# Kernel tuning notes

Hardware: AMD Instinct MI355X
Metric: run time of the kernel (lower is better)

## Reference

```python
import jax, jax.numpy as jnp
import numpy as np

D_MODEL = 512
NUM_HEADS = 8
HEAD_DIM = D_MODEL // NUM_HEADS
MAX_REL = 2


def setup_inputs() -> dict:
    key = jax.random.key(0)
    ks = jax.random.split(key, 12)
    B, S = 2, 4096
    std = 1.0 / np.sqrt(D_MODEL)
    inp = {
        'q': jax.random.normal(ks[0], (B, S, D_MODEL), jnp.float32),
        'k': jax.random.normal(ks[1], (B, S, D_MODEL), jnp.float32),
        'v': jax.random.normal(ks[2], (B, S, D_MODEL), jnp.float32),
        'Wq': jax.random.normal(ks[3], (D_MODEL, D_MODEL), jnp.float32) * std,
        'bq': jnp.zeros((D_MODEL,), jnp.float32),
        'Wk': jax.random.normal(ks[4], (D_MODEL, D_MODEL), jnp.float32) * std,
        'bk': jnp.zeros((D_MODEL,), jnp.float32),
        'Wv': jax.random.normal(ks[5], (D_MODEL, D_MODEL), jnp.float32) * std,
        'bv': jnp.zeros((D_MODEL,), jnp.float32),
        'Wo': jax.random.normal(ks[6], (D_MODEL, D_MODEL), jnp.float32) * std,
        'bo': jnp.zeros((D_MODEL,), jnp.float32),
        'rel_pos': jax.random.normal(ks[7], (NUM_HEADS, 2 * MAX_REL + 1), jnp.float32),
    }
    return inp


def _rel_bias(rel_pos, seq_len):
    pos = jnp.arange(seq_len)
    rel = pos[None, :] - pos[:, None]              # [S,S]
    idx = jnp.clip(rel, -MAX_REL, MAX_REL) + MAX_REL
    return rel_pos[:, idx]                         # [H,S,S]


def reference(q, k, v, Wq, bq, Wk, bk, Wv, bv, Wo, bo, rel_pos):
    B, S, D = q.shape
    H, Hd = NUM_HEADS, HEAD_DIM
    # torch Linear: x @ W.T + b
    Q = (q @ Wq.T + bq).reshape(B, S, H, Hd).transpose(0, 2, 1, 3)  # [B,H,S,Hd]
    K = (k @ Wk.T + bk).reshape(B, S, H, Hd).transpose(0, 2, 1, 3)
    V = (v @ Wv.T + bv).reshape(B, S, H, Hd).transpose(0, 2, 1, 3)
    scores = jnp.einsum('bhqd,bhkd->bhqk', Q, K) / jnp.sqrt(jnp.float32(Hd))
    scores = scores + _rel_bias(rel_pos, S)[None]                  # [B,H,S,S]
    probs = jax.nn.softmax(scores, axis=-1)
    attn = jnp.einsum('bhqk,bhkd->bhqd', probs, V)                 # [B,H,S,Hd]
    attn = attn.transpose(0, 2, 1, 3).reshape(B, S, D)
    return attn @ Wo.T + bo
```

## Files before the change

kernel.cpp:

```cpp
#include <hip/hip_runtime.h>

typedef __bf16 bf16_t;
typedef __bf16 bf16x2 __attribute__((ext_vector_type(2)));
typedef __bf16 bf16x4 __attribute__((ext_vector_type(4)));
typedef __bf16 bf16x8 __attribute__((ext_vector_type(8)));
typedef float f32x4 __attribute__((ext_vector_type(4)));
typedef unsigned int u32x4 __attribute__((ext_vector_type(4)));

#define MFMA16(a, b, c) __builtin_amdgcn_mfma_f32_16x16x32_bf16(a, b, c, 0, 0, 0)
#define LOG2E 1.4426950408889634f
#define SHIFT 16.0f

#define GLL(g, l)                                                      \
  __builtin_amdgcn_global_load_lds(                                    \
      (const __attribute__((address_space(1))) void*)(g),              \
      (__attribute__((address_space(3))) void*)(l), 16, 0, 0)

#define WAIT_BARRIER_V4() asm volatile("s_waitcnt vmcnt(4)\n\ts_barrier" ::: "memory")
#define WAIT_BARRIER_V6() asm volatile("s_waitcnt vmcnt(6)\n\ts_barrier" ::: "memory")
#define WAIT_BARRIER_V8() asm volatile("s_waitcnt vmcnt(8)\n\ts_barrier" ::: "memory")

static constexpr int NB = 2;
static constexpr int SEQ = 4096;
static constexpr int DM = 512;
static constexpr int NH = 8;
static constexpr int HD = 64;
static constexpr int M_ROWS = NB * SEQ;

__global__ __launch_bounds__(256) void cvt_w_kernel(
    const float* __restrict__ w0, const float* __restrict__ w1,
    const float* __restrict__ w2, const float* __restrict__ w3,
    bf16_t* __restrict__ out) {
  const float* src = (blockIdx.y == 0) ? w0 : (blockIdx.y == 1) ? w1
                   : (blockIdx.y == 2) ? w2 : w3;
  int i = (blockIdx.x * 256 + threadIdx.x) * 4;
  float4 v = *(const float4*)(src + i);
  bf16_t* o = out + blockIdx.y * (DM * DM) + i;
  o[0] = (bf16_t)v.x; o[1] = (bf16_t)v.y; o[2] = (bf16_t)v.z; o[3] = (bf16_t)v.w;
}

__global__ __launch_bounds__(256) void cvt_x_kernel(
    const float* __restrict__ q, const float* __restrict__ k,
    const float* __restrict__ v, bf16_t* __restrict__ out) {
  const float* src = (blockIdx.y == 0) ? q : (blockIdx.y == 1) ? k : v;
  bf16_t* dst = out + (size_t)blockIdx.y * (M_ROWS * DM);
  int i = (blockIdx.x * 256 + threadIdx.x) * 8;
  float4 a = *(const float4*)(src + i);
  float4 b = *(const float4*)(src + i + 4);
  bf16x8 o;
  o[0] = (bf16_t)a.x; o[1] = (bf16_t)a.y; o[2] = (bf16_t)a.z; o[3] = (bf16_t)a.w;
  o[4] = (bf16_t)b.x; o[5] = (bf16_t)b.y; o[6] = (bf16_t)b.z; o[7] = (bf16_t)b.w;
  *(bf16x8*)(dst + i) = o;
}

__device__ __forceinline__ void gemm_body64(
    const bf16_t* __restrict__ X, const bf16_t* __restrict__ Wm,
    const float* __restrict__ bias, void* __restrict__ Out,
    int omode, float scale) {
  __shared__ bf16_t Asm[3][64 * 64];
  __shared__ bf16_t Bsm[3][128 * 64];

  const int tid = threadIdx.x;
  const int w = tid >> 6;
  const int lane = tid & 63;
  const int quad = lane >> 4, l15 = lane & 15;
  const int l8 = lane >> 3;
  const int swcol = ((lane & 7) ^ l8) * 8;
  const int m0 = blockIdx.x * 64;
  const int n0 = blockIdx.y * 128;
  const int moff = (w & 1) * 32;
  const int noff = (w >> 1) * 64;

  f32x4 acc[2][4];
#pragma unroll
  for (int mb = 0; mb < 2; mb++)
#pragma unroll
    for (int nb = 0; nb < 4; nb++) { acc[mb][nb][0] = 0.f; acc[mb][nb][1] = 0.f; acc[mb][nb][2] = 0.f; acc[mb][nb][3] = 0.f; }

  auto stage = [&](int ks, int bufi) {
    const int k0 = ks * 64;
#pragma unroll
    for (int j = 0; j < 4; j++) {
      const int row = j * 32 + w * 8 + l8;
      GLL(Wm + (size_t)(n0 + row) * DM + k0 + swcol, &Bsm[bufi][(j * 256 + w * 64) * 8]);
    }
#pragma unroll
    for (int j = 0; j < 2; j++) {
      const int row = j * 32 + w * 8 + l8;
      GLL(X + (size_t)(m0 + row) * DM + k0 + swcol, &Asm[bufi][(j * 256 + w * 64) * 8]);
    }
  };

  stage(0, 0);
  stage(1, 1);

  for (int ks = 0; ks < 8; ks++) {
    WAIT_BARRIER_V6();
    const int tn = (ks + 2 < 8) ? ks + 2 : 7;
    stage(tn, (ks + 2) % 3);
    const int p = ks % 3;

#pragma unroll
    for (int kd = 0; kd < 2; kd++) {
      const int fch = (((kd << 2) + quad) ^ (l15 & 7)) << 3;
      bf16x8 bfr[4];
#pragma unroll
      for (int nb = 0; nb < 4; nb++)
        bfr[nb] = *(const bf16x8*)&Bsm[p][(noff + nb * 16 + l15) * 64 + fch];
#pragma unroll
      for (int mb = 0; mb < 2; mb++) {
        bf16x8 a = *(const bf16x8*)&Asm[p][(moff + mb * 16 + l15) * 64 + fch];
#pragma unroll
        for (int nb = 0; nb < 4; nb++) acc[mb][nb] = MFMA16(a, bfr[nb], acc[mb][nb]);
      }
    }
  }

#pragma unroll
  for (int nb = 0; nb < 4; nb++) {
    const int n = n0 + noff + nb * 16 + l15;
    const float bn = bias[n];
    const int h = n >> 6, dd = n & 63;
#pragma unroll
    for (int mb = 0; mb < 2; mb++) {
      const int mbase = m0 + moff + mb * 16 + quad * 4;
      const int bb = mbase >> 12, s = mbase & 4095;
      if (omode == 0) {
#pragma unroll
        for (int r = 0; r < 4; r++) {
          const float val = (acc[mb][nb][r] + bn) * scale;
          ((bf16_t*)Out)[(size_t)((bb * NH + h) * SEQ + s + r) * HD + dd] = (bf16_t)val;
        }
      } else if (omode == 1) {
        bf16x4 pk;
#pragma unroll
        for (int r = 0; r < 4; r++) pk[r] = (bf16_t)(acc[mb][nb][r] + bn);
        *(bf16x4*)&((bf16_t*)Out)[(((size_t)(bb * NH + h) * HD + dd) << 12) + s] = pk;
      } else {
#pragma unroll
        for (int r = 0; r < 4; r++)
          ((float*)Out)[(size_t)(mbase + r) * DM + n] = acc[mb][nb][r] + bn;
      }
    }
  }
}

__global__ __launch_bounds__(256, 2) void qkv_kernel(
    const bf16_t* __restrict__ Xall, const bf16_t* __restrict__ Wall,
    const float* __restrict__ bq, const float* __restrict__ bk,
    const float* __restrict__ bv, bf16_t* __restrict__ Qb,
    bf16_t* __restrict__ Kb, bf16_t* __restrict__ Vb, float qscale) {
  const int z = blockIdx.z;
  const bf16_t* X = Xall + (size_t)z * (M_ROWS * DM);
  const float* bias = (z == 0) ? bq : (z == 1) ? bk : bv;
  bf16_t* Out = (z == 0) ? Qb : (z == 1) ? Kb : Vb;
  gemm_body64(X, Wall + (size_t)z * DM * DM, bias, Out,
              (z == 2) ? 1 : 0, (z == 0) ? qscale : 1.0f);
}

__global__ __launch_bounds__(256, 2) void oproj_kernel(
    const bf16_t* __restrict__ X, const bf16_t* __restrict__ Wm,
    const float* __restrict__ bias, float* __restrict__ Out) {
  gemm_body64(X, Wm, bias, Out, 2, 1.0f);
}

__global__ __launch_bounds__(256, 2) void attn_kernel(
    const bf16_t* __restrict__ Qb, const bf16_t* __restrict__ Kb,
    const bf16_t* __restrict__ Vb, const float* __restrict__ rel_pos,
    bf16_t* __restrict__ attn_out) {
  __shared__ bf16_t Kt[4][64 * 64];
  __shared__ bf16_t Vt[4][64 * 64];

  const int tid = threadIdx.x;
  const int w = tid >> 6;
  const int lane = tid & 63;
  const int quad = lane >> 4, l15 = lane & 15;

  const int lin = blockIdx.x;
  const int glob = (lin & 7) * 64 + (lin >> 3);
  const int bh = glob >> 5;
  const int qb = glob & 31;
  const int b = bh >> 3, h = bh & 7;
  const int qlo = qb * 128 + w * 32;

  const float rb0 = rel_pos[h * 5 + 0] * LOG2E;
  const float rb1 = rel_pos[h * 5 + 1] * LOG2E;
  const float rb2 = rel_pos[h * 5 + 2] * LOG2E;
  const float rb3 = rel_pos[h * 5 + 3] * LOG2E;
  const float rb4 = rel_pos[h * 5 + 4] * LOG2E;

  bf16x8 qf[2][2];
#pragma unroll
  for (int mb = 0; mb < 2; mb++)
#pragma unroll
    for (int kd = 0; kd < 2; kd++)
      qf[mb][kd] = *(const bf16x8*)(Qb + (size_t)(bh * SEQ + qlo + mb * 16 + l15) * HD + kd * 32 + 8 * quad);

  f32x4 o[2][4];
#pragma unroll
  for (int mb = 0; mb < 2; mb++)
#pragma unroll
    for (int db = 0; db < 4; db++) { o[mb][db][0] = 0.f; o[mb][db][1] = 0.f; o[mb][db][2] = 0.f; o[mb][db][3] = 0.f; }
  f32x4 l4[2];
  l4[0][0] = 0.f; l4[0][1] = 0.f; l4[0][2] = 0.f; l4[0][3] = 0.f;
  l4[1][0] = 0.f; l4[1][1] = 0.f; l4[1][2] = 0.f; l4[1][3] = 0.f;

  bf16x8 ones;
#pragma unroll
  for (int i = 0; i < 8; i++) ones[i] = (bf16_t)1.0f;

  const int srow = (w << 4) + (lane >> 3);
  const int scol = (((lane & 7) ^ (lane >> 3)) << 3);
  const bf16_t* kg0 = Kb + ((size_t)(bh * SEQ + srow) << 6) + scol;
  const bf16_t* vg0 = Vb + (((size_t)(bh * HD + srow)) << 12) + scol;
  const int ldst = (w << 10);

  const int sw = l15 & 7;
  const int kfo0 = (l15 << 6) + ((quad ^ sw) << 3);
  const int kfo1 = (l15 << 6) + (((quad + 4) ^ sw) << 3);

  auto stage = [&](int t, int bufi) {
    GLL(kg0 + ((size_t)t << 12), &Kt[bufi][ldst]);
    GLL(kg0 + ((size_t)t << 12) + (8 << 6), &Kt[bufi][ldst + 512]);
    GLL(vg0 + (t << 6), &Vt[bufi][ldst]);
    GLL(vg0 + (t << 6) + (8 << 12), &Vt[bufi][ldst + 512]);
  };

  auto qk_tile = [&](int tq, f32x4 (&s)[2][4]) {
    const int kk0 = tq * 64;
    float cini;
    if (kk0 >= qlo + 33)            cini = rb4 - SHIFT;
    else if (kk0 + 63 <= qlo - 2)   cini = rb0 - SHIFT;
    else                            cini = -SHIFT;
#pragma unroll
    for (int mb = 0; mb < 2; mb++)
#pragma unroll
      for (int kb = 0; kb < 4; kb++) { s[mb][kb][0] = cini; s[mb][kb][1] = cini; s[mb][kb][2] = cini; s[mb][kb][3] = cini; }
    const int pq = tq & 3;
    __builtin_amdgcn_s_setprio(1);
#pragma unroll
    for (int kb = 0; kb < 4; kb++) {
      bf16x8 kA0 = *(const bf16x8*)&Kt[pq][kfo0 + (kb << 10)];
      bf16x8 kA1 = *(const bf16x8*)&Kt[pq][kfo1 + (kb << 10)];
      s[0][kb] = MFMA16(kA0, qf[0][0], s[0][kb]);
      s[0][kb] = MFMA16(kA1, qf[0][1], s[0][kb]);
      s[1][kb] = MFMA16(kA0, qf[1][0], s[1][kb]);
      s[1][kb] = MFMA16(kA1, qf[1][1], s[1][kb]);
    }
    __builtin_amdgcn_s_setprio(0);
  };

  auto sm_pv = [&](int t, f32x4 (&s)[2][4]) {
    const int kk0 = t * 64;
    const bool nearband = !(kk0 >= qlo + 33) && !(kk0 + 63 <= qlo - 2);
    if (nearband) {
#pragma unroll
      for (int mb = 0; mb < 2; mb++) {
        const int qg = qlo + mb * 16 + l15;
#pragma unroll
        for (int kb = 0; kb < 4; kb++)
#pragma unroll
          for (int r = 0; r < 4; r++) {
            int dl = kk0 + kb * 16 + quad * 4 + r - qg;
            float bias = dl <= -2 ? rb0
                       : (dl >= 2 ? rb4
                       : (dl == -1 ? rb1 : (dl == 0 ? rb2 : rb3)));
            s[mb][kb][r] += bias;
          }
      }
    }

    bf16x8 pf[2][2];
#pragma unroll
    for (int mb = 0; mb < 2; mb++) {
      unsigned int u[4][2];
#pragma unroll
      for (int kb = 0; kb < 4; kb++) {
        bf16x2 p0, p1;
        p0[0] = (bf16_t)__builtin_amdgcn_exp2f(s[mb][kb][0]);
        p0[1] = (bf16_t)__builtin_amdgcn_exp2f(s[mb][kb][1]);
        p1[0] = (bf16_t)__builtin_amdgcn_exp2f(s[mb][kb][2]);
        p1[1] = (bf16_t)__builtin_amdgcn_exp2f(s[mb][kb][3]);
        u[kb][0] = __builtin_bit_cast(unsigned int, p0);
        u[kb][1] = __builtin_bit_cast(unsigned int, p1);
      }
#pragma unroll
      for (int kc = 0; kc < 2; kc++) {
        unsigned int a0 = u[2 * kc][0], b0 = u[2 * kc + 1][0];
        unsigned int a1 = u[2 * kc][1], b1 = u[2 * kc + 1][1];
        asm("v_permlane32_swap_b32 %0, %1" : "+v"(a0), "+v"(b0));
        asm("v_permlane32_swap_b32 %0, %1" : "+v"(a1), "+v"(b1));
        asm("v_permlane16_swap_b32 %0, %1" : "+v"(a0), "+v"(b0));
        asm("v_permlane16_swap_b32 %0, %1" : "+v"(a1), "+v"(b1));
        u32x4 pk; pk[0] = a0; pk[1] = a1; pk[2] = b0; pk[3] = b1;
        pf[mb][kc] = __builtin_bit_cast(bf16x8, pk);
      }
    }

    const int p = t & 3;
    __builtin_amdgcn_s_setprio(1);
    l4[0] = MFMA16(ones, pf[0][0], l4[0]);
    l4[0] = MFMA16(ones, pf[0][1], l4[0]);
    l4[1] = MFMA16(ones, pf[1][0], l4[1]);
    l4[1] = MFMA16(ones, pf[1][1], l4[1]);
#pragma unroll
    for (int db = 0; db < 4; db++) {
      bf16x8 vA0 = *(const bf16x8*)&Vt[p][kfo0 + (db << 10)];
      bf16x8 vA1 = *(const bf16x8*)&Vt[p][kfo1 + (db << 10)];
      o[0][db] = MFMA16(vA0, pf[0][0], o[0][db]);
      o[0][db] = MFMA16(vA1, pf[0][1], o[0][db]);
      o[1][db] = MFMA16(vA0, pf[1][0], o[1][db]);
      o[1][db] = MFMA16(vA1, pf[1][1], o[1][db]);
    }
    __builtin_amdgcn_s_setprio(0);
  };

  stage(0, 0);
  stage(1, 1);
  stage(2, 2);
  WAIT_BARRIER_V8();

  f32x4 sA[2][4], sB[2][4];
  qk_tile(0, sA);

  for (int t2 = 0; t2 < 32; t2++) {
    {
      const int t = 2 * t2;
      WAIT_BARRIER_V4();
      const int tg = (t + 3 < 64) ? t + 3 : 63;
      stage(tg, (t + 3) & 3);
      qk_tile(t + 1, sB);
      sm_pv(t, sA);
    }
    {
      const int t = 2 * t2 + 1;
      WAIT_BARRIER_V4();
      const int tg = (t + 3 < 64) ? t + 3 : 63;
      stage(tg, (t + 3) & 3);
      if (t < 63) qk_tile(t + 1, sA);
      sm_pv(t, sB);
    }
  }

#pragma unroll
  for (int mb = 0; mb < 2; mb++) {
    const float inv = 1.0f / l4[mb][0];
    const int qg = qlo + mb * 16 + l15;
#pragma unroll
    for (int db = 0; db < 4; db++) {
      bf16x4 pk;
#pragma unroll
      for (int r = 0; r < 4; r++) pk[r] = (bf16_t)(o[mb][db][r] * inv);
      *(bf16x4*)(attn_out + (size_t)(b * SEQ + qg) * DM + h * HD + db * 16 + quad * 4) = pk;
    }
  }
}

extern "C" void kernel_launch(void* const* d_in, const int* in_sizes, int n_in,
                              void* d_out, int out_size, void* d_ws, size_t ws_size,
                              hipStream_t stream) {
  const float* q   = (const float*)d_in[0];
  const float* k   = (const float*)d_in[1];
  const float* v   = (const float*)d_in[2];
  const float* Wq  = (const float*)d_in[3];
  const float* bq  = (const float*)d_in[4];
  const float* Wk  = (const float*)d_in[5];
  const float* bk  = (const float*)d_in[6];
  const float* Wv  = (const float*)d_in[7];
  const float* bv  = (const float*)d_in[8];
  const float* Wo  = (const float*)d_in[9];
  const float* bo  = (const float*)d_in[10];
  const float* rel = (const float*)d_in[11];

  char* ws = (char*)d_ws;
  bf16_t* Wbf  = (bf16_t*)ws;
  bf16_t* Xb   = (bf16_t*)(ws + (size_t)(2  << 20));
  bf16_t* Qbuf = (bf16_t*)(ws + (size_t)(26 << 20));
  bf16_t* Kbuf = (bf16_t*)(ws + (size_t)(34 << 20));
  bf16_t* Vbuf = (bf16_t*)(ws + (size_t)(42 << 20));
  bf16_t* Abuf = (bf16_t*)(ws + (size_t)(2  << 20));

  cvt_w_kernel<<<dim3(256, 4), 256, 0, stream>>>(Wq, Wk, Wv, Wo, Wbf);
  cvt_x_kernel<<<dim3(2048, 3), 256, 0, stream>>>(q, k, v, Xb);

  const float qscale = LOG2E / 8.0f;
  qkv_kernel<<<dim3(128, 4, 3), 256, 0, stream>>>(
      Xb, Wbf, bq, bk, bv, Qbuf, Kbuf, Vbuf, qscale);

  attn_kernel<<<512, 256, 0, stream>>>(Qbuf, Kbuf, Vbuf, rel, Abuf);

  oproj_kernel<<<dim3(128, 4), 256, 0, stream>>>(Abuf, Wbf + 3 * DM * DM, bo, (float*)d_out);
}
```

Before: 232.7 us.

## Split attention waves into 2x2 query/key grid with cross-wave reduction

Each wave now handles 64 query rows over half of each 64-key tile instead of 32 query rows over the full tile. K and V fragments loaded from LDS are reused across four query blocks instead of two, which halves the LDS fragment reads per MFMA. The two key-half partial outputs and row sums are combined through shared memory at the end. In exchange, accumulator registers per wave grow, and an extra LDS reduction with two barriers is added.

```diff
diff --git a/kernel.cpp b/kernel.cpp
--- a/kernel.cpp
+++ b/kernel.cpp
@@ -175,13 +175,14 @@
   const int w = tid >> 6;
   const int lane = tid & 63;
   const int quad = lane >> 4, l15 = lane & 15;
+  const int wq = w >> 1, wk = w & 1;
 
   const int lin = blockIdx.x;
   const int glob = (lin & 7) * 64 + (lin >> 3);
   const int bh = glob >> 5;
   const int qb = glob & 31;
   const int b = bh >> 3, h = bh & 7;
-  const int qlo = qb * 128 + w * 32;
+  const int qlo = qb * 128 + wq * 64;
 
   const float rb0 = rel_pos[h * 5 + 0] * LOG2E;
   const float rb1 = rel_pos[h * 5 + 1] * LOG2E;
@@ -189,21 +190,21 @@
   const float rb3 = rel_pos[h * 5 + 3] * LOG2E;
   const float rb4 = rel_pos[h * 5 + 4] * LOG2E;
 
-  bf16x8 qf[2][2];
-#pragma unroll
-  for (int mb = 0; mb < 2; mb++)
+  bf16x8 qf[4][2];
+#pragma unroll
+  for (int mb = 0; mb < 4; mb++)
 #pragma unroll
     for (int kd = 0; kd < 2; kd++)
       qf[mb][kd] = *(const bf16x8*)(Qb + (size_t)(bh * SEQ + qlo + mb * 16 + l15) * HD + kd * 32 + 8 * quad);
 
-  f32x4 o[2][4];
-#pragma unroll
-  for (int mb = 0; mb < 2; mb++)
+  f32x4 o[4][4];
+#pragma unroll
+  for (int mb = 0; mb < 4; mb++)
 #pragma unroll
     for (int db = 0; db < 4; db++) { o[mb][db][0] = 0.f; o[mb][db][1] = 0.f; o[mb][db][2] = 0.f; o[mb][db][3] = 0.f; }
-  f32x4 l4[2];
-  l4[0][0] = 0.f; l4[0][1] = 0.f; l4[0][2] = 0.f; l4[0][3] = 0.f;
-  l4[1][0] = 0.f; l4[1][1] = 0.f; l4[1][2] = 0.f; l4[1][3] = 0.f;
+  f32x4 l4[4];
+#pragma unroll
+  for (int mb = 0; mb < 4; mb++) { l4[mb][0] = 0.f; l4[mb][1] = 0.f; l4[mb][2] = 0.f; l4[mb][3] = 0.f; }
 
   bf16x8 ones;
 #pragma unroll
@@ -218,6 +219,8 @@
   const int sw = l15 & 7;
   const int kfo0 = (l15 << 6) + ((quad ^ sw) << 3);
   const int kfo1 = (l15 << 6) + (((quad + 4) ^ sw) << 3);
+  const int vfo = (l15 << 6) + ((((wk << 2) + quad) ^ sw) << 3);
+  const int wk2 = wk << 1;
 
   auto stage = [&](int t, int bufi) {
     GLL(kg0 + ((size_t)t << 12), &Kt[bufi][ldst]);
@@ -226,42 +229,46 @@
     GLL(vg0 + (t << 6) + (8 << 12), &Vt[bufi][ldst + 512]);
   };
 
-  auto qk_tile = [&](int tq, f32x4 (&s)[2][4]) {
-    const int kk0 = tq * 64;
+  auto qk_tile = [&](int tq, f32x4 (&s)[4][2]) {
+    const int klo = tq * 64 + wk * 32;
     float cini;
-    if (kk0 >= qlo + 33)            cini = rb4 - SHIFT;
-    else if (kk0 + 63 <= qlo - 2)   cini = rb0 - SHIFT;
-    else                            cini = -SHIFT;
-#pragma unroll
-    for (int mb = 0; mb < 2; mb++)
-#pragma unroll
-      for (int kb = 0; kb < 4; kb++) { s[mb][kb][0] = cini; s[mb][kb][1] = cini; s[mb][kb][2] = cini; s[mb][kb][3] = cini; }
+    if (klo >= qlo + 65)        cini = rb4 - SHIFT;
+    else if (klo <= qlo - 33)   cini = rb0 - SHIFT;
+    else                        cini = -SHIFT;
+#pragma unroll
+    for (int mb = 0; mb < 4; mb++)
+#pragma unroll
+      for (int kb = 0; kb < 2; kb++) { s[mb][kb][0] = cini; s[mb][kb][1] = cini; s[mb][kb][2] = cini; s[mb][kb][3] = cini; }
     const int pq = tq & 3;
     __builtin_amdgcn_s_setprio(1);
 #pragma unroll
-    for (int kb = 0; kb < 4; kb++) {
-      bf16x8 kA0 = *(const bf16x8*)&Kt[pq][kfo0 + (kb << 10)];
-      bf16x8 kA1 = *(const bf16x8*)&Kt[pq][kfo1 + (kb << 10)];
+    for (int kb = 0; kb < 2; kb++) {
+      bf16x8 kA0 = *(const bf16x8*)&Kt[pq][kfo0 + ((wk2 + kb) << 10)];
+      bf16x8 kA1 = *(const bf16x8*)&Kt[pq][kfo1 + ((wk2 + kb) << 10)];
       s[0][kb] = MFMA16(kA0, qf[0][0], s[0][kb]);
       s[0][kb] = MFMA16(kA1, qf[0][1], s[0][kb]);
       s[1][kb] = MFMA16(kA0, qf[1][0], s[1][kb]);
       s[1][kb] = MFMA16(kA1, qf[1][1], s[1][kb]);
+      s[2][kb] = MFMA16(kA0, qf[2][0], s[2][kb]);
+      s[2][kb] = MFMA16(kA1, qf[2][1], s[2][kb]);
+      s[3][kb] = MFMA16(kA0, qf[3][0], s[3][kb]);
+      s[3][kb] = MFMA16(kA1, qf[3][1], s[3][kb]);
     }
     __builtin_amdgcn_s_setprio(0);
   };
 
-  auto sm_pv = [&](int t, f32x4 (&s)[2][4]) {
-    const int kk0 = t * 64;
-    const bool nearband = !(kk0 >= qlo + 33) && !(kk0 + 63 <= qlo - 2);
+  auto sm_pv = [&](int t, f32x4 (&s)[4][2]) {
+    const int klo = t * 64 + wk * 32;
+    const bool nearband = !(klo >= qlo + 65) && !(klo <= qlo - 33);
     if (nearband) {
 #pragma unroll
-      for (int mb = 0; mb < 2; mb++) {
+      for (int mb = 0; mb < 4; mb++) {
         const int qg = qlo + mb * 16 + l15;
 #pragma unroll
-        for (int kb = 0; kb < 4; kb++)
+        for (int kb = 0; kb < 2; kb++)
 #pragma unroll
           for (int r = 0; r < 4; r++) {
-            int dl = kk0 + kb * 16 + quad * 4 + r - qg;
+            int dl = klo + kb * 16 + quad * 4 + r - qg;
             float bias = dl <= -2 ? rb0
                        : (dl >= 2 ? rb4
                        : (dl == -1 ? rb1 : (dl == 0 ? rb2 : rb3)));
@@ -270,12 +277,12 @@
       }
     }
 
-    bf16x8 pf[2][2];
-#pragma unroll
-    for (int mb = 0; mb < 2; mb++) {
-      unsigned int u[4][2];
-#pragma unroll
-      for (int kb = 0; kb < 4; kb++) {
+    bf16x8 pf[4];
+#pragma unroll
+    for (int mb = 0; mb < 4; mb++) {
+      unsigned int u[2][2];
+#pragma unroll
+      for (int kb = 0; kb < 2; kb++) {
         bf16x2 p0, p1;
         p0[0] = (bf16_t)__builtin_amdgcn_exp2f(s[mb][kb][0]);
         p0[1] = (bf16_t)__builtin_amdgcn_exp2f(s[mb][kb][1]);
@@ -284,33 +291,29 @@
         u[kb][0] = __builtin_bit_cast(unsigned int, p0);
         u[kb][1] = __builtin_bit_cast(unsigned int, p1);
       }
-#pragma unroll
-      for (int kc = 0; kc < 2; kc++) {
-        unsigned int a0 = u[2 * kc][0], b0 = u[2 * kc + 1][0];
-        unsigned int a1 = u[2 * kc][1], b1 = u[2 * kc + 1][1];
-        asm("v_permlane32_swap_b32 %0, %1" : "+v"(a0), "+v"(b0));
-        asm("v_permlane32_swap_b32 %0, %1" : "+v"(a1), "+v"(b1));
-        asm("v_permlane16_swap_b32 %0, %1" : "+v"(a0), "+v"(b0));
-        asm("v_permlane16_swap_b32 %0, %1" : "+v"(a1), "+v"(b1));
-        u32x4 pk; pk[0] = a0; pk[1] = a1; pk[2] = b0; pk[3] = b1;
-        pf[mb][kc] = __builtin_bit_cast(bf16x8, pk);
-      }
+      unsigned int a0 = u[0][0], b0 = u[1][0];
+      unsigned int a1 = u[0][1], b1 = u[1][1];
+      asm("v_permlane32_swap_b32 %0, %1" : "+v"(a0), "+v"(b0));
+      asm("v_permlane32_swap_b32 %0, %1" : "+v"(a1), "+v"(b1));
+      asm("v_permlane16_swap_b32 %0, %1" : "+v"(a0), "+v"(b0));
+      asm("v_permlane16_swap_b32 %0, %1" : "+v"(a1), "+v"(b1));
+      u32x4 pk; pk[0] = a0; pk[1] = a1; pk[2] = b0; pk[3] = b1;
+      pf[mb] = __builtin_bit_cast(bf16x8, pk);
     }
 
     const int p = t & 3;
     __builtin_amdgcn_s_setprio(1);
-    l4[0] = MFMA16(ones, pf[0][0], l4[0]);
-    l4[0] = MFMA16(ones, pf[0][1], l4[0]);
-    l4[1] = MFMA16(ones, pf[1][0], l4[1]);
-    l4[1] = MFMA16(ones, pf[1][1], l4[1]);
+    l4[0] = MFMA16(ones, pf[0], l4[0]);
+    l4[1] = MFMA16(ones, pf[1], l4[1]);
+    l4[2] = MFMA16(ones, pf[2], l4[2]);
+    l4[3] = MFMA16(ones, pf[3], l4[3]);
 #pragma unroll
     for (int db = 0; db < 4; db++) {
-      bf16x8 vA0 = *(const bf16x8*)&Vt[p][kfo0 + (db << 10)];
-      bf16x8 vA1 = *(const bf16x8*)&Vt[p][kfo1 + (db << 10)];
-      o[0][db] = MFMA16(vA0, pf[0][0], o[0][db]);
-      o[0][db] = MFMA16(vA1, pf[0][1], o[0][db]);
-      o[1][db] = MFMA16(vA0, pf[1][0], o[1][db]);
-      o[1][db] = MFMA16(vA1, pf[1][1], o[1][db]);
+      bf16x8 vA = *(const bf16x8*)&Vt[p][vfo + (db << 10)];
+      o[0][db] = MFMA16(vA, pf[0], o[0][db]);
+      o[1][db] = MFMA16(vA, pf[1], o[1][db]);
+      o[2][db] = MFMA16(vA, pf[2], o[2][db]);
+      o[3][db] = MFMA16(vA, pf[3], o[3][db]);
     }
     __builtin_amdgcn_s_setprio(0);
   };
@@ -320,7 +323,7 @@
   stage(2, 2);
   WAIT_BARRIER_V8();
 
-  f32x4 sA[2][4], sB[2][4];
+  f32x4 sA[4][2], sB[4][2];
   qk_tile(0, sA);
 
   for (int t2 = 0; t2 < 32; t2++) {
@@ -342,16 +345,37 @@
     }
   }
 
-#pragma unroll
-  for (int mb = 0; mb < 2; mb++) {
-    const float inv = 1.0f / l4[mb][0];
-    const int qg = qlo + mb * 16 + l15;
-#pragma unroll
-    for (int db = 0; db < 4; db++) {
-      bf16x4 pk;
-#pragma unroll
-      for (int r = 0; r < 4; r++) pk[r] = (bf16_t)(o[mb][db][r] * inv);
-      *(bf16x4*)(attn_out + (size_t)(b * SEQ + qg) * DM + h * HD + db * 16 + quad * 4) = pk;
+  asm volatile("s_waitcnt vmcnt(0)" ::: "memory");
+  __syncthreads();
+  float* Ored = (float*)&Kt[0][0];
+  float* lred = (float*)&Vt[0][0];
+  if (wk) {
+#pragma unroll
+    for (int mb = 0; mb < 4; mb++) {
+      lred[(wq << 6) + (mb << 4) + l15] = l4[mb][0];
+#pragma unroll
+      for (int db = 0; db < 4; db++) {
+        const int ch = ((db << 2) | quad) ^ sw;
+        *(f32x4*)&Ored[(wq << 12) + ((mb * 16 + l15) << 6) + (ch << 2)] = o[mb][db];
+      }
+    }
+  }
+  __syncthreads();
+  if (!wk) {
+#pragma unroll
+    for (int mb = 0; mb < 4; mb++) {
+      float lsum = l4[mb][0] + lred[(wq << 6) + (mb << 4) + l15];
+      const float inv = 1.0f / lsum;
+      const int qg = qlo + mb * 16 + l15;
+#pragma unroll
+      for (int db = 0; db < 4; db++) {
+        const int ch = ((db << 2) | quad) ^ sw;
+        const f32x4 part = *(const f32x4*)&Ored[(wq << 12) + ((mb * 16 + l15) << 6) + (ch << 2)];
+        bf16x4 pk;
+#pragma unroll
+        for (int r = 0; r < 4; r++) pk[r] = (bf16_t)((o[mb][db][r] + part[r]) * inv);
+        *(bf16x4*)(attn_out + (size_t)(b * SEQ + qg) * DM + h * HD + db * 16 + quad * 4) = pk;
+      }
     }
   }
 }
```

Measured after the change: 230.8 us. About the same (-0.8%).
